# Optimization experiments

Hardware: AMD Instinct MI355X
Metric: run time of the kernel (lower is better)

The kernel has to match this reference:

```python
import jax, jax.numpy as jnp
import numpy as np

B, N, K, F = 32, 4096, 20, 64


def setup_inputs() -> dict:
    key = jax.random.key(0)
    k1, k2 = jax.random.split(key)
    topk_indices = jax.random.randint(k1, (B, N, K), 0, N, dtype=jnp.int32)
    features = jax.random.normal(k2, (B, N, F), dtype=jnp.float32)
    return {"topk_indices": topk_indices, "features": features}


def reference(topk_indices, features):
    # Equivalent of tf.gather_nd with [batch_idx, point_idx] pairs:
    # out[b, n, k, :] = features[b, topk_indices[b, n, k], :]
    batch_idx = jnp.arange(features.shape[0])[:, None, None]  # [B,1,1]
    return features[batch_idx, topk_indices]  # [B, N, K, F]
```

## Files before the change

### kernel.cpp

```cpp
#include <hip/hip_runtime.h>


constexpr int B = 32, N = 4096, K = 20, F = 64;
constexpr unsigned TOTAL_ROWS = (unsigned)B * N * K;
constexpr unsigned VEC_PER_ROW = F / 4;
constexpr unsigned TOTAL_VEC = TOTAL_ROWS * VEC_PER_ROW;
constexpr unsigned NK = (unsigned)N * K;

constexpr unsigned BLOCK = 256;
constexpr unsigned GRID = 2048;
constexpr unsigned THREADS = GRID * BLOCK;
constexpr unsigned ITERS = TOTAL_VEC / THREADS;
static_assert(ITERS * THREADS == TOTAL_VEC, "exact tiling");

__global__ __launch_bounds__(BLOCK) void gather_rows_kernel(
    const int* __restrict__ idx,
    const float* __restrict__ feat,
    float* __restrict__ out)
{
    unsigned i = blockIdx.x * BLOCK + threadIdx.x;
    const float4* __restrict__ featv = reinterpret_cast<const float4*>(feat);
    float4* __restrict__ outv = reinterpret_cast<float4*>(out);

#pragma unroll 4
    for (unsigned j = 0; j < ITERS; ++j, i += THREADS) {
        unsigned row = i >> 4;
        unsigned v   = i & 15u;
        unsigned b   = row / NK;
        int id       = idx[row];
        unsigned src = (b * (unsigned)N + (unsigned)id) * VEC_PER_ROW + v;
        outv[i] = featv[src];
    }
}

extern "C" void kernel_launch(void* const* d_in, const int* in_sizes, int n_in,
                              void* d_out, int out_size, void* d_ws, size_t ws_size,
                              hipStream_t stream) {
    const int*   idx  = (const int*)d_in[0];
    const float* feat = (const float*)d_in[1];
    float*       out  = (float*)d_out;

    gather_rows_kernel<<<GRID, BLOCK, 0, stream>>>(idx, feat, out);
}
```

Before: 207.7 us.

## Map batches to XCDs so each batch's feature slab stays in one L2

```diff
diff --git a/kernel.cpp b/kernel.cpp
--- a/kernel.cpp
+++ b/kernel.cpp
@@ -2,34 +2,41 @@
 
 
 constexpr int B = 32, N = 4096, K = 20, F = 64;
-constexpr unsigned TOTAL_ROWS = (unsigned)B * N * K;
-constexpr unsigned VEC_PER_ROW = F / 4;
-constexpr unsigned TOTAL_VEC = TOTAL_ROWS * VEC_PER_ROW;
 constexpr unsigned NK = (unsigned)N * K;
+constexpr unsigned F4_PER_FEAT_BATCH = (unsigned)N * F / 4;
+constexpr unsigned F4_PER_BATCH = NK * (F / 4);
 
 constexpr unsigned BLOCK = 256;
-constexpr unsigned GRID = 2048;
-constexpr unsigned THREADS = GRID * BLOCK;
-constexpr unsigned ITERS = TOTAL_VEC / THREADS;
-static_assert(ITERS * THREADS == TOTAL_VEC, "exact tiling");
+constexpr unsigned CHUNKS_PER_BATCH = 256;
+constexpr unsigned GRID = (unsigned)B * CHUNKS_PER_BATCH;
+constexpr unsigned F4_PER_CHUNK = F4_PER_BATCH / CHUNKS_PER_BATCH;
+constexpr unsigned ITERS = F4_PER_CHUNK / BLOCK;
+static_assert(ITERS * BLOCK * CHUNKS_PER_BATCH == F4_PER_BATCH, "exact tiling");
 
 __global__ __launch_bounds__(BLOCK) void gather_rows_kernel(
     const int* __restrict__ idx,
     const float* __restrict__ feat,
     float* __restrict__ out)
 {
-    unsigned i = blockIdx.x * BLOCK + threadIdx.x;
+    const unsigned xcd = blockIdx.x & 7u;
+    const unsigned seq = blockIdx.x >> 3;
+    const unsigned b   = xcd + 8u * (seq >> 8);
+    const unsigned c   = seq & 255u;
+
     const float4* __restrict__ featv = reinterpret_cast<const float4*>(feat);
     float4* __restrict__ outv = reinterpret_cast<float4*>(out);
 
-#pragma unroll 4
-    for (unsigned j = 0; j < ITERS; ++j, i += THREADS) {
-        unsigned row = i >> 4;
-        unsigned v   = i & 15u;
-        unsigned b   = row / NK;
-        int id       = idx[row];
-        unsigned src = (b * (unsigned)N + (unsigned)id) * VEC_PER_ROW + v;
-        outv[i] = featv[src];
+    const int* __restrict__ idxb = idx + b * NK;
+    const unsigned featbase = b * F4_PER_FEAT_BATCH;
+    const unsigned outbase  = b * F4_PER_BATCH;
+
+#pragma unroll 1
+    for (unsigned j = 0; j < ITERS; ++j) {
+        unsigned il  = c * F4_PER_CHUNK + j * BLOCK + threadIdx.x;
+        unsigned row = il >> 4;
+        unsigned v   = il & 15u;
+        int id       = idxb[row];
+        outv[outbase + il] = featv[featbase + ((unsigned)id << 4) + v];
     }
 }
 
```

Result: faster. 186.3 us (median of 2 runs) (-10.3%).
